# Optimization experiments

Measured on AMD Instinct MI355X. Metric: run time of the kernel, lower is better.

Reference implementation:

```python
import jax, jax.numpy as jnp
import numpy as np

N_NODES = 50000
N_EDGES = 600000
HIDDEN = 128
EDGE_NF = 2          # concat([radial, edge_attr]) -> edges_in_d = 2
NORM_FACTOR = 100.0  # normalization_factor, aggregation 'sum'
NORM_CONSTANT = 1.0


def _lin(key, out_d, in_d):
    # xavier-ish init, (out, in) layout like torch.nn.Linear
    return jax.random.normal(key, (out_d, in_d), jnp.float32) * (1.0 / np.sqrt(in_d))


def setup_inputs() -> dict:
    key = jax.random.key(0)
    ks = iter(jax.random.split(key, 64))
    H = HIDDEN
    inp = {
        "h": jax.random.normal(next(ks), (N_NODES, H), jnp.float32),
        "x": jax.random.normal(next(ks), (N_NODES, 3), jnp.float32),
        "edge_attr": jax.random.normal(next(ks), (N_EDGES, 1), jnp.float32),
        "edge_index": jax.random.randint(next(ks), (2, N_EDGES), 0, N_NODES),
    }
    for i in range(2):  # two GCL layers
        inp[f"g{i}_ew1"] = _lin(next(ks), H, 2 * H + EDGE_NF)
        inp[f"g{i}_eb1"] = jnp.zeros((H,), jnp.float32)
        inp[f"g{i}_ew2"] = _lin(next(ks), H, H)
        inp[f"g{i}_eb2"] = jnp.zeros((H,), jnp.float32)
        inp[f"g{i}_aw"] = _lin(next(ks), 1, H)
        inp[f"g{i}_ab"] = jnp.zeros((1,), jnp.float32)
        inp[f"g{i}_nw1"] = _lin(next(ks), H, 2 * H)
        inp[f"g{i}_nb1"] = jnp.zeros((H,), jnp.float32)
        inp[f"g{i}_nw2"] = _lin(next(ks), H, H)
        inp[f"g{i}_nb2"] = jnp.zeros((H,), jnp.float32)
    inp["eq_w1"] = _lin(next(ks), H, 2 * H + EDGE_NF)
    inp["eq_b1"] = jnp.zeros((H,), jnp.float32)
    inp["eq_w2"] = _lin(next(ks), H, H)
    inp["eq_b2"] = jnp.zeros((H,), jnp.float32)
    inp["eq_w3"] = _lin(next(ks), 1, H)  # bias=False
    return inp


def reference(h, x, edge_attr, edge_index,
              g0_ew1, g0_eb1, g0_ew2, g0_eb2, g0_aw, g0_ab, g0_nw1, g0_nb1, g0_nw2, g0_nb2,
              g1_ew1, g1_eb1, g1_ew2, g1_eb2, g1_aw, g1_ab, g1_nw1, g1_nb1, g1_nw2, g1_nb2,
              eq_w1, eq_b1, eq_w2, eq_b2, eq_w3):
    silu = jax.nn.silu
    row, col = edge_index[0], edge_index[1]
    n = h.shape[0]

    # coord2diff
    diff = x[row] - x[col]                                   # [E, 3]
    radial = jnp.sum(diff * diff, axis=1, keepdims=True)     # [E, 1]
    norm = jnp.sqrt(radial + 1e-8)
    coord_diff = diff / (norm + NORM_CONSTANT)
    ea = jnp.concatenate([radial, edge_attr], axis=1)        # [E, 2]

    gcls = [
        (g0_ew1, g0_eb1, g0_ew2, g0_eb2, g0_aw, g0_ab, g0_nw1, g0_nb1, g0_nw2, g0_nb2),
        (g1_ew1, g1_eb1, g1_ew2, g1_eb2, g1_aw, g1_ab, g1_nw1, g1_nb1, g1_nw2, g1_nb2),
    ]
    for (ew1, eb1, ew2, eb2, aw, ab, nw1, nb1, nw2, nb2) in gcls:
        # edge model: gather -> MLP -> attention gate
        e_in = jnp.concatenate([h[row], h[col], ea], axis=1)  # [E, 2H+2]
        mij = silu(silu(e_in @ ew1.T + eb1) @ ew2.T + eb2)    # [E, H]
        att = jax.nn.sigmoid(mij @ aw.T + ab)                 # [E, 1]
        ef = mij * att
        # node model: scatter-add (sum agg, / normalization_factor)
        agg = jax.ops.segment_sum(ef, row, num_segments=n) / NORM_FACTOR
        msg = silu(jnp.concatenate([h, agg], axis=1) @ nw1.T + nb1) @ nw2.T + nb2
        h = h + msg

    # EquivariantUpdate (tanh=False)
    e_in = jnp.concatenate([h[row], h[col], ea], axis=1)
    s = silu(silu(e_in @ eq_w1.T + eq_b1) @ eq_w2.T + eq_b2) @ eq_w3.T  # [E, 1]
    trans = coord_diff * s                                              # [E, 3]
    x = x + jax.ops.segment_sum(trans, row, num_segments=n) / NORM_FACTOR
    return (h, x)
```

## Files before the change

kernel.cpp:

```cpp
#include <hip/hip_runtime.h>
#include <cmath>

typedef short bfv8 __attribute__((ext_vector_type(8)));
typedef float fv4  __attribute__((ext_vector_type(4)));

#define MFMA_B16(a,b,c) __builtin_amdgcn_mfma_f32_16x16x32_bf16((a),(b),(c),0,0,0)

__device__ __forceinline__ float siluf(float x) { return x / (1.0f + expf(-x)); }

__device__ __forceinline__ unsigned packsplit(float v) {
  unsigned uh = __float_as_uint(v) & 0xffff0000u;
  float lof = v - __uint_as_float(uh);
  return (uh >> 16) | (__float_as_uint(lof) & 0xffff0000u);
}

template <int MODE>
__global__ __launch_bounds__(256, 3)
void edge_mfma(const unsigned short* __restrict__ hhi,
               const unsigned short* __restrict__ hlo,
               const float* __restrict__ radial,
               const float* __restrict__ eattr,
               const int* __restrict__ eidx, int E,
               const unsigned short* __restrict__ w1h, const unsigned short* __restrict__ w1l,
               const float* __restrict__ W1full, const float* __restrict__ b1,
               const unsigned short* __restrict__ w2h, const unsigned short* __restrict__ w2l,
               const float* __restrict__ b2,
               const float* __restrict__ awv, const float* __restrict__ abv,
               const float* __restrict__ xin,
               float* __restrict__ outbuf)
{
  __shared__ int   sRow[128], sCol[128];
  __shared__ float sRad[128], sEa[128];
  __shared__ __align__(16) unsigned sH[4][2048];

  const int tid = threadIdx.x;
  const int w = tid >> 6, l = tid & 63;
  const int c16 = l & 15, g = l >> 4;
  const int e0 = blockIdx.x * 128;

  if (tid < 128) {
    int e = min(e0 + tid, E - 1);
    sRow[tid] = eidx[e];
    sCol[tid] = eidx[E + e];
    sRad[tid] = radial[e];
    sEa[tid]  = eattr[e];
  }
  __syncthreads();

  const int rw = w * 32;
  int nidA[2], nidB[2];
#pragma unroll
  for (int rt = 0; rt < 2; ++rt) {
    nidA[rt] = sRow[rw + rt * 16 + c16];
    nidB[rt] = sCol[rw + rt * 16 + c16];
  }

  fv4 acc[2][8];
#pragma unroll
  for (int a = 0; a < 2; ++a)
#pragma unroll
    for (int b = 0; b < 8; ++b) acc[a][b] = (fv4)0.0f;

#pragma unroll 2
  for (int kc = 0; kc < 8; ++kc) {
    bfv8 Ah[2], Al[2];
    const int kh = (kc & 3) * 32 + g * 8;
#pragma unroll
    for (int rt = 0; rt < 2; ++rt) {
      const int nid = (kc < 4) ? nidA[rt] : nidB[rt];
      const size_t off = (size_t)nid * 128 + kh;
      Ah[rt] = *(const bfv8*)(hhi + off);
      Al[rt] = *(const bfv8*)(hlo + off);
    }
#pragma unroll
    for (int jt = 0; jt < 8; ++jt) {
      const size_t bo = ((size_t)(kc * 8 + jt) * 64 + l) * 8;
      bfv8 Bh = *(const bfv8*)(w1h + bo);
      bfv8 Bl = *(const bfv8*)(w1l + bo);
#pragma unroll
      for (int rt = 0; rt < 2; ++rt) {
        acc[rt][jt] = MFMA_B16(Ah[rt], Bh, acc[rt][jt]);
        acc[rt][jt] = MFMA_B16(Al[rt], Bh, acc[rt][jt]);
        acc[rt][jt] = MFMA_B16(Ah[rt], Bl, acc[rt][jt]);
      }
    }
  }

  unsigned* sHW = sH[w];
  const float ab0 = (MODE == 0) ? abv[0] : 0.0f;

#pragma unroll 1
  for (int rt = 0; rt < 2; ++rt) {
#pragma unroll
    for (int jt = 0; jt < 8; ++jt) {
      const int col = jt * 16 + c16;
      const float wt0 = W1full[(size_t)col * 258 + 256];
      const float wt1 = W1full[(size_t)col * 258 + 257];
      const float bb  = b1[col];
#pragma unroll
      for (int reg = 0; reg < 4; ++reg) {
        const int rr = 4 * g + reg;
        const int er = rw + rt * 16 + rr;
        const float v = acc[rt][jt][reg] + sRad[er] * wt0 + sEa[er] * wt1 + bb;
        sHW[rr * 128 + (col ^ ((rr & 7) << 2))] = packsplit(siluf(v));
      }
    }

    fv4 accB[8];
#pragma unroll
    for (int jt = 0; jt < 8; ++jt) accB[jt] = (fv4)0.0f;
    const int sxz = (c16 & 7) << 2;
#pragma unroll 2
    for (int kc2 = 0; kc2 < 4; ++kc2) {
      const int k0 = kc2 * 32 + g * 8;
      const int i1 = c16 * 128 + (k0 ^ sxz);
      const int4 q0 = *((const int4*)(sHW + i1));
      const int4 q1 = *((const int4*)(sHW + (i1 ^ 4)));
      bfv8 Ah2, Al2;
      {
        const int qq[8] = {q0.x, q0.y, q0.z, q0.w, q1.x, q1.y, q1.z, q1.w};
#pragma unroll
        for (int i = 0; i < 8; ++i) {
          Ah2[i] = (short)(((unsigned)qq[i]) & 0xffffu);
          Al2[i] = (short)(((unsigned)qq[i]) >> 16);
        }
      }
#pragma unroll
      for (int jt = 0; jt < 8; ++jt) {
        const size_t bo = ((size_t)(kc2 * 8 + jt) * 64 + l) * 8;
        bfv8 Bh = *(const bfv8*)(w2h + bo);
        bfv8 Bl = *(const bfv8*)(w2l + bo);
        accB[jt] = MFMA_B16(Ah2, Bh, accB[jt]);
        accB[jt] = MFMA_B16(Al2, Bh, accB[jt]);
        accB[jt] = MFMA_B16(Ah2, Bl, accB[jt]);
      }
    }

    float p[4] = {0.f, 0.f, 0.f, 0.f};
#pragma unroll
    for (int jt = 0; jt < 8; ++jt) {
      const int col = jt * 16 + c16;
      const float bb = b2[col], aa = awv[col];
#pragma unroll
      for (int reg = 0; reg < 4; ++reg) {
        const float m = siluf(accB[jt][reg] + bb);
        accB[jt][reg] = m;
        p[reg] += m * aa;
      }
    }
#pragma unroll
    for (int msk = 1; msk < 16; msk <<= 1) {
#pragma unroll
      for (int reg = 0; reg < 4; ++reg) p[reg] += __shfl_xor(p[reg], msk, 64);
    }

    if constexpr (MODE == 0) {
#pragma unroll
      for (int reg = 0; reg < 4; ++reg) {
        const int er = rw + rt * 16 + 4 * g + reg;
        const int e = e0 + er;
        if (e < E) {
          const float att = 1.0f / (1.0f + expf(-(p[reg] + ab0)));
          float* dst = outbuf + (size_t)sRow[er] * 128;
#pragma unroll
          for (int jt = 0; jt < 8; ++jt)
            unsafeAtomicAdd(dst + jt * 16 + c16, accB[jt][reg] * att);
        }
      }
    } else {
      if (c16 == 0) {
#pragma unroll
        for (int reg = 0; reg < 4; ++reg) {
          const int er = rw + rt * 16 + 4 * g + reg;
          const int e = e0 + er;
          if (e < E) {
            const float s = p[reg] * 0.01f;
            const int nr = sRow[er], nc = sCol[er];
            const float dx = xin[(size_t)nr * 3 + 0] - xin[(size_t)nc * 3 + 0];
            const float dy = xin[(size_t)nr * 3 + 1] - xin[(size_t)nc * 3 + 1];
            const float dz = xin[(size_t)nr * 3 + 2] - xin[(size_t)nc * 3 + 2];
            const float inv = 1.0f / (sqrtf(dx * dx + dy * dy + dz * dz + 1e-8f) + 1.0f);
            unsafeAtomicAdd(outbuf + (size_t)nr * 3 + 0, dx * inv * s);
            unsafeAtomicAdd(outbuf + (size_t)nr * 3 + 1, dy * inv * s);
            unsafeAtomicAdd(outbuf + (size_t)nr * 3 + 2, dz * inv * s);
          }
        }
      }
    }
  }
}

__global__ __launch_bounds__(256, 3)
void node_mfma(float* __restrict__ hio,
               const unsigned short* __restrict__ hhi,
               const unsigned short* __restrict__ hlo,
               const float* __restrict__ agg, int N,
               const unsigned short* __restrict__ w1h, const unsigned short* __restrict__ w1l,
               const float* __restrict__ b1,
               const unsigned short* __restrict__ w2h, const unsigned short* __restrict__ w2l,
               const float* __restrict__ b2)
{
  __shared__ __align__(16) unsigned sH[4][2048];

  const int tid = threadIdx.x;
  const int w = tid >> 6, l = tid & 63;
  const int c16 = l & 15, g = l >> 4;
  const int n0 = blockIdx.x * 128;
  const int rw = w * 32;

  int rowA[2];
#pragma unroll
  for (int rt = 0; rt < 2; ++rt) rowA[rt] = min(n0 + rw + rt * 16 + c16, N - 1);

  fv4 acc[2][8];
#pragma unroll
  for (int a = 0; a < 2; ++a)
#pragma unroll
    for (int b = 0; b < 8; ++b) acc[a][b] = (fv4)0.0f;

#pragma unroll 2
  for (int kc = 0; kc < 8; ++kc) {
    bfv8 Ah[2], Al[2];
    if (kc < 4) {
      const int kh = kc * 32 + g * 8;
#pragma unroll
      for (int rt = 0; rt < 2; ++rt) {
        const size_t off = (size_t)rowA[rt] * 128 + kh;
        Ah[rt] = *(const bfv8*)(hhi + off);
        Al[rt] = *(const bfv8*)(hlo + off);
      }
    } else {
      const int kh = (kc - 4) * 32 + g * 8;
#pragma unroll
      for (int rt = 0; rt < 2; ++rt) {
        const float4 v0 = *(const float4*)(agg + (size_t)rowA[rt] * 128 + kh);
        const float4 v1 = *(const float4*)(agg + (size_t)rowA[rt] * 128 + kh + 4);
        const float vv[8] = {v0.x, v0.y, v0.z, v0.w, v1.x, v1.y, v1.z, v1.w};
#pragma unroll
        for (int i = 0; i < 8; ++i) {
          const float xs = vv[i] * 0.01f;
          const unsigned uh = __float_as_uint(xs) & 0xffff0000u;
          Ah[rt][i] = (short)(uh >> 16);
          const float lof = xs - __uint_as_float(uh);
          Al[rt][i] = (short)(__float_as_uint(lof) >> 16);
        }
      }
    }
#pragma unroll
    for (int jt = 0; jt < 8; ++jt) {
      const size_t bo = ((size_t)(kc * 8 + jt) * 64 + l) * 8;
      bfv8 Bh = *(const bfv8*)(w1h + bo);
      bfv8 Bl = *(const bfv8*)(w1l + bo);
#pragma unroll
      for (int rt = 0; rt < 2; ++rt) {
        acc[rt][jt] = MFMA_B16(Ah[rt], Bh, acc[rt][jt]);
        acc[rt][jt] = MFMA_B16(Al[rt], Bh, acc[rt][jt]);
        acc[rt][jt] = MFMA_B16(Ah[rt], Bl, acc[rt][jt]);
      }
    }
  }

  unsigned* sHW = sH[w];
#pragma unroll 1
  for (int rt = 0; rt < 2; ++rt) {
#pragma unroll
    for (int jt = 0; jt < 8; ++jt) {
      const int col = jt * 16 + c16;
      const float bb = b1[col];
#pragma unroll
      for (int reg = 0; reg < 4; ++reg) {
        const int rr = 4 * g + reg;
        sHW[rr * 128 + (col ^ ((rr & 7) << 2))] = packsplit(siluf(acc[rt][jt][reg] + bb));
      }
    }

    fv4 accB[8];
#pragma unroll
    for (int jt = 0; jt < 8; ++jt) accB[jt] = (fv4)0.0f;
    const int sxz = (c16 & 7) << 2;
#pragma unroll 2
    for (int kc2 = 0; kc2 < 4; ++kc2) {
      const int k0 = kc2 * 32 + g * 8;
      const int i1 = c16 * 128 + (k0 ^ sxz);
      const int4 q0 = *((const int4*)(sHW + i1));
      const int4 q1 = *((const int4*)(sHW + (i1 ^ 4)));
      bfv8 Ah2, Al2;
      {
        const int qq[8] = {q0.x, q0.y, q0.z, q0.w, q1.x, q1.y, q1.z, q1.w};
#pragma unroll
        for (int i = 0; i < 8; ++i) {
          Ah2[i] = (short)(((unsigned)qq[i]) & 0xffffu);
          Al2[i] = (short)(((unsigned)qq[i]) >> 16);
        }
      }
#pragma unroll
      for (int jt = 0; jt < 8; ++jt) {
        const size_t bo = ((size_t)(kc2 * 8 + jt) * 64 + l) * 8;
        bfv8 Bh = *(const bfv8*)(w2h + bo);
        bfv8 Bl = *(const bfv8*)(w2l + bo);
        accB[jt] = MFMA_B16(Ah2, Bh, accB[jt]);
        accB[jt] = MFMA_B16(Al2, Bh, accB[jt]);
        accB[jt] = MFMA_B16(Ah2, Bl, accB[jt]);
      }
    }

#pragma unroll
    for (int reg = 0; reg < 4; ++reg) {
      const int n = n0 + rw + rt * 16 + 4 * g + reg;
      if (n < N) {
        float* hp = hio + (size_t)n * 128;
#pragma unroll
        for (int jt = 0; jt < 8; ++jt) {
          const int col = jt * 16 + c16;
          hp[col] += accB[jt][reg] + b2[col];
        }
      }
    }
  }
}

__global__ void radial_kernel(const float* __restrict__ x,
                              const int* __restrict__ eidx, int E,
                              float* __restrict__ radial)
{
  const int e = blockIdx.x * 256 + threadIdx.x;
  if (e >= E) return;
  const int r = eidx[e], c = eidx[E + e];
  const float dx = x[(size_t)r * 3 + 0] - x[(size_t)c * 3 + 0];
  const float dy = x[(size_t)r * 3 + 1] - x[(size_t)c * 3 + 1];
  const float dz = x[(size_t)r * 3 + 2] - x[(size_t)c * 3 + 2];
  radial[e] = dx * dx + dy * dy + dz * dz;
}

__global__ void split_kernel(const float* __restrict__ src,
                             unsigned short* __restrict__ hi,
                             unsigned short* __restrict__ lo, int n4)
{
  const int i = blockIdx.x * 256 + threadIdx.x;
  if (i >= n4) return;
  const float4 v = ((const float4*)src)[i];
  const float vv[4] = {v.x, v.y, v.z, v.w};
  ushort4 ho, lq;
  unsigned short* hp = (unsigned short*)&ho;
  unsigned short* lp = (unsigned short*)&lq;
#pragma unroll
  for (int k = 0; k < 4; ++k) {
    const unsigned uh = __float_as_uint(vv[k]) & 0xffff0000u;
    hp[k] = (unsigned short)(uh >> 16);
    const float lof = vv[k] - __uint_as_float(uh);
    lp[k] = (unsigned short)(__float_as_uint(lof) >> 16);
  }
  ((ushort4*)hi)[i] = ho;
  ((ushort4*)lo)[i] = lq;
}

struct WDesc { const float* src; unsigned short* hi; unsigned short* lo; int K; int SW; };
struct WAll { WDesc m[10]; };

__global__ void wprep_kernel(WAll wa)
{
  const WDesc d = wa.m[blockIdx.y];
  const int idx = blockIdx.x * 256 + threadIdx.x;
  const int j = idx & 127, k = idx >> 7;
  if (k >= d.K) return;
  const float v = d.src[(size_t)j * d.SW + k];
  const unsigned uh = __float_as_uint(v) & 0xffff0000u;
  const float lof = v - __uint_as_float(uh);
  const int fo = ((((k >> 5) * 8 + (j >> 4)) * 64) + ((k >> 3) & 3) * 16 + (j & 15)) * 8 + (k & 7);
  d.hi[fo] = (unsigned short)(uh >> 16);
  d.lo[fo] = (unsigned short)(__float_as_uint(lof) >> 16);
}

extern "C" void kernel_launch(void* const* d_in, const int* in_sizes, int n_in,
                              void* d_out, int out_size, void* d_ws, size_t ws_size,
                              hipStream_t stream)
{
  const float* h_in  = (const float*)d_in[0];
  const float* x_in  = (const float*)d_in[1];
  const float* eattr = (const float*)d_in[2];
  const int*   eidx  = (const int*)d_in[3];
  const int N = in_sizes[0] / 128;
  const int E = in_sizes[2];

  const float* P[25];
  for (int i = 0; i < 25; ++i) P[i] = (const float*)d_in[4 + i];

  float* h_out = (float*)d_out;
  float* x_out = (float*)d_out + (size_t)N * 128;

  float* radial = (float*)d_ws;
  float* agg    = radial + E;
  unsigned short* hhi = (unsigned short*)(agg + (size_t)N * 128);
  unsigned short* hlo = hhi + (size_t)N * 128;
  unsigned short* wptr = hlo + (size_t)N * 128;

  WAll wa;
  auto addw = [&](int slot, const float* s, int K, int SW) {
    wa.m[slot].src = s; wa.m[slot].hi = wptr; wa.m[slot].lo = wptr + (size_t)K * 128;
    wa.m[slot].K = K; wa.m[slot].SW = SW;
    wptr += (size_t)2 * K * 128;
  };
  addw(0, P[0], 256, 258);  addw(1, P[2], 128, 128);
  addw(2, P[6], 256, 256);  addw(3, P[8], 128, 128);
  addw(4, P[10], 256, 258); addw(5, P[12], 128, 128);
  addw(6, P[16], 256, 256); addw(7, P[18], 128, 128);
  addw(8, P[20], 256, 258); addw(9, P[22], 128, 128);

  hipMemcpyAsync(h_out, h_in, (size_t)N * 128 * sizeof(float),
                 hipMemcpyDeviceToDevice, stream);
  hipMemcpyAsync(x_out, x_in, (size_t)N * 3 * sizeof(float),
                 hipMemcpyDeviceToDevice, stream);

  radial_kernel<<<(E + 255) / 256, 256, 0, stream>>>(x_in, eidx, E, radial);
  wprep_kernel<<<dim3(128, 10), 256, 0, stream>>>(wa);

  const int n4 = N * 32;
  const int sg = (n4 + 255) / 256;
  const int eg = (E + 127) / 128;
  const int ng = (N + 127) / 128;

  for (int lyr = 0; lyr < 2; ++lyr) {
    const float* const* G = P + 10 * lyr;
    const WDesc* M = &wa.m[4 * lyr];
    split_kernel<<<sg, 256, 0, stream>>>(h_out, hhi, hlo, n4);
    hipMemsetAsync(agg, 0, (size_t)N * 128 * sizeof(float), stream);
    edge_mfma<0><<<eg, 256, 0, stream>>>(hhi, hlo, radial, eattr, eidx, E,
        M[0].hi, M[0].lo, G[0], G[1], M[1].hi, M[1].lo, G[3],
        G[4], G[5], nullptr, agg);
    node_mfma<<<ng, 256, 0, stream>>>(h_out, hhi, hlo, agg, N,
        M[2].hi, M[2].lo, G[7], M[3].hi, M[3].lo, G[9]);
  }

  split_kernel<<<sg, 256, 0, stream>>>(h_out, hhi, hlo, n4);
  edge_mfma<1><<<eg, 256, 0, stream>>>(hhi, hlo, radial, eattr, eidx, E,
      wa.m[8].hi, wa.m[8].lo, P[20], P[21], wa.m[9].hi, wa.m[9].lo, P[23],
      P[24], nullptr, x_in, x_out);
}
```

Before: 1.565 ms.

## Sort edges by destination row and pre-reduce messages in LDS before atomics

Adds a counting sort (histogram, scan, scatter) that reorders edges by row, and fuses the radial computation into the scatter step. In the message-passing edge kernel, per-edge messages are staged in shared memory as bf16 pairs, then summed over runs of equal row before any global atomic, so far fewer atomics hit agg. The point is to cut atomic traffic, which dominates the scatter-add. The costs are extra preprocessing kernels, a larger shared-memory footprint with occupancy hint lowered to 2, and bf16 rounding of messages before accumulation, which reduces precision.

```diff
diff --git a/kernel.cpp b/kernel.cpp
--- a/kernel.cpp
+++ b/kernel.cpp
@@ -14,13 +14,73 @@
   return (uh >> 16) | (__float_as_uint(lof) & 0xffff0000u);
 }
 
+__device__ __forceinline__ unsigned bf16rne(float x) {
+  unsigned u = __float_as_uint(x);
+  return (u + 0x7fffu + ((u >> 16) & 1u)) >> 16;
+}
+
+__global__ void hist_kernel(const int* __restrict__ eidx, int E,
+                            unsigned* __restrict__ cnt)
+{
+  const int e = blockIdx.x * 256 + threadIdx.x;
+  if (e < E) atomicAdd(&cnt[eidx[e]], 1u);
+}
+
+__global__ void scan_kernel(const unsigned* __restrict__ cnt,
+                            unsigned* __restrict__ cursor, int N)
+{
+  __shared__ unsigned part[1024];
+  const int t = threadIdx.x;
+  const int chunk = (N + 1023) / 1024;
+  const int base = t * chunk;
+  unsigned s = 0;
+  for (int i = 0; i < chunk; ++i) {
+    const int idx = base + i;
+    if (idx < N) s += cnt[idx];
+  }
+  part[t] = s;
+  __syncthreads();
+  for (int off = 1; off < 1024; off <<= 1) {
+    unsigned v = 0;
+    if (t >= off) v = part[t - off];
+    __syncthreads();
+    if (t >= off) part[t] += v;
+    __syncthreads();
+  }
+  unsigned pre = (t == 0) ? 0u : part[t - 1];
+  for (int i = 0; i < chunk; ++i) {
+    const int idx = base + i;
+    if (idx < N) { cursor[idx] = pre; pre += cnt[idx]; }
+  }
+}
+
+__global__ void scatter_kernel(const float* __restrict__ x,
+                               const int* __restrict__ eidx,
+                               const float* __restrict__ eattr, int E,
+                               unsigned* __restrict__ cursor,
+                               int* __restrict__ sRowA, int* __restrict__ sColA,
+                               float* __restrict__ sRadA, float* __restrict__ sEaA)
+{
+  const int e = blockIdx.x * 256 + threadIdx.x;
+  if (e >= E) return;
+  const int r = eidx[e], c = eidx[E + e];
+  const float dx = x[(size_t)r * 3 + 0] - x[(size_t)c * 3 + 0];
+  const float dy = x[(size_t)r * 3 + 1] - x[(size_t)c * 3 + 1];
+  const float dz = x[(size_t)r * 3 + 2] - x[(size_t)c * 3 + 2];
+  const unsigned pos = atomicAdd(&cursor[r], 1u);
+  sRowA[pos] = r;
+  sColA[pos] = c;
+  sRadA[pos] = dx * dx + dy * dy + dz * dz;
+  sEaA[pos]  = eattr[e];
+}
+
 template <int MODE>
-__global__ __launch_bounds__(256, 3)
+__global__ __launch_bounds__(256, 2)
 void edge_mfma(const unsigned short* __restrict__ hhi,
                const unsigned short* __restrict__ hlo,
-               const float* __restrict__ radial,
-               const float* __restrict__ eattr,
-               const int* __restrict__ eidx, int E,
+               const int* __restrict__ sRowA, const int* __restrict__ sColA,
+               const float* __restrict__ sRadA, const float* __restrict__ sEaA,
+               int E,
                const unsigned short* __restrict__ w1h, const unsigned short* __restrict__ w1l,
                const float* __restrict__ W1full, const float* __restrict__ b1,
                const unsigned short* __restrict__ w2h, const unsigned short* __restrict__ w2l,
@@ -29,9 +89,14 @@
                const float* __restrict__ xin,
                float* __restrict__ outbuf)
 {
-  __shared__ int   sRow[128], sCol[128];
-  __shared__ float sRad[128], sEa[128];
-  __shared__ __align__(16) unsigned sH[4][2048];
+  extern __shared__ __align__(16) char smem[];
+  unsigned* sHall  = (unsigned*)smem;
+  unsigned* sStage = (unsigned*)(smem + 32768);
+  char* ebase = smem + (MODE == 0 ? 65536 : 32768);
+  int*   sRow = (int*)ebase;
+  int*   sCol = sRow + 128;
+  float* sRad = (float*)(sCol + 128);
+  float* sEa  = sRad + 128;
 
   const int tid = threadIdx.x;
   const int w = tid >> 6, l = tid & 63;
@@ -39,11 +104,11 @@
   const int e0 = blockIdx.x * 128;
 
   if (tid < 128) {
-    int e = min(e0 + tid, E - 1);
-    sRow[tid] = eidx[e];
-    sCol[tid] = eidx[E + e];
-    sRad[tid] = radial[e];
-    sEa[tid]  = eattr[e];
+    const int e = min(e0 + tid, E - 1);
+    sRow[tid] = sRowA[e];
+    sCol[tid] = sColA[e];
+    sRad[tid] = sRadA[e];
+    sEa[tid]  = sEaA[e];
   }
   __syncthreads();
 
@@ -86,7 +151,7 @@
     }
   }
 
-  unsigned* sHW = sH[w];
+  unsigned* sHW = sHall + w * 2048;
   const float ab0 = (MODE == 0) ? abv[0] : 0.0f;
 
 #pragma unroll 1
@@ -155,16 +220,22 @@
     }
 
     if constexpr (MODE == 0) {
-#pragma unroll
-      for (int reg = 0; reg < 4; ++reg) {
-        const int er = rw + rt * 16 + 4 * g + reg;
-        const int e = e0 + er;
-        if (e < E) {
-          const float att = 1.0f / (1.0f + expf(-(p[reg] + ab0)));
-          float* dst = outbuf + (size_t)sRow[er] * 128;
-#pragma unroll
-          for (int jt = 0; jt < 8; ++jt)
-            unsafeAtomicAdd(dst + jt * 16 + c16, accB[jt][reg] * att);
+      float att[4];
+#pragma unroll
+      for (int reg = 0; reg < 4; ++reg)
+        att[reg] = 1.0f / (1.0f + expf(-(p[reg] + ab0)));
+#pragma unroll
+      for (int jt = 0; jt < 8; ++jt) {
+#pragma unroll
+        for (int reg = 0; reg < 4; ++reg) {
+          const int er = rw + rt * 16 + 4 * g + reg;
+          float v = (e0 + er < E) ? accB[jt][reg] * att[reg] : 0.0f;
+          const float vn = __shfl_xor(v, 1, 64);
+          if (!(c16 & 1)) {
+            const int cp = jt * 8 + (c16 >> 1);
+            sStage[er * 64 + (cp ^ (((er >> 2) & 3) << 3))] =
+                bf16rne(v) | (bf16rne(vn) << 16);
+          }
         }
       }
     } else {
@@ -188,6 +259,34 @@
       }
     }
   }
+
+  if constexpr (MODE == 0) {
+    __syncthreads();
+    const int cp = tid & 63;
+    const int q  = tid >> 6;
+    const int erb = q * 32;
+    float a0 = 0.0f, a1 = 0.0f;
+    int cur = sRow[erb];
+#pragma unroll 4
+    for (int i = 0; i < 32; ++i) {
+      const int er = erb + i;
+      const int r = sRow[er];
+      if (r != cur) {
+        if (a0 != 0.0f || a1 != 0.0f) {
+          unsafeAtomicAdd(outbuf + (size_t)cur * 128 + 2 * cp,     a0);
+          unsafeAtomicAdd(outbuf + (size_t)cur * 128 + 2 * cp + 1, a1);
+        }
+        cur = r; a0 = 0.0f; a1 = 0.0f;
+      }
+      const unsigned u = sStage[er * 64 + (cp ^ (((er >> 2) & 3) << 3))];
+      a0 += __uint_as_float(u << 16);
+      a1 += __uint_as_float(u & 0xffff0000u);
+    }
+    if (a0 != 0.0f || a1 != 0.0f) {
+      unsafeAtomicAdd(outbuf + (size_t)cur * 128 + 2 * cp,     a0);
+      unsafeAtomicAdd(outbuf + (size_t)cur * 128 + 2 * cp + 1, a1);
+    }
+  }
 }
 
 __global__ __launch_bounds__(256, 3)
@@ -319,19 +418,6 @@
   }
 }
 
-__global__ void radial_kernel(const float* __restrict__ x,
-                              const int* __restrict__ eidx, int E,
-                              float* __restrict__ radial)
-{
-  const int e = blockIdx.x * 256 + threadIdx.x;
-  if (e >= E) return;
-  const int r = eidx[e], c = eidx[E + e];
-  const float dx = x[(size_t)r * 3 + 0] - x[(size_t)c * 3 + 0];
-  const float dy = x[(size_t)r * 3 + 1] - x[(size_t)c * 3 + 1];
-  const float dz = x[(size_t)r * 3 + 2] - x[(size_t)c * 3 + 2];
-  radial[e] = dx * dx + dy * dy + dz * dz;
-}
-
 __global__ void split_kernel(const float* __restrict__ src,
                              unsigned short* __restrict__ hi,
                              unsigned short* __restrict__ lo, int n4)
@@ -388,9 +474,14 @@
   float* h_out = (float*)d_out;
   float* x_out = (float*)d_out + (size_t)N * 128;
 
-  float* radial = (float*)d_ws;
-  float* agg    = radial + E;
-  unsigned short* hhi = (unsigned short*)(agg + (size_t)N * 128);
+  float*    agg    = (float*)d_ws;
+  unsigned* cnt    = (unsigned*)(agg + (size_t)N * 128);
+  unsigned* cursor = cnt + N;
+  int*      sRowA  = (int*)(cursor + N);
+  int*      sColA  = sRowA + E;
+  float*    sRadA  = (float*)(sColA + E);
+  float*    sEaA   = sRadA + E;
+  unsigned short* hhi = (unsigned short*)(sEaA + E);
   unsigned short* hlo = hhi + (size_t)N * 128;
   unsigned short* wptr = hlo + (size_t)N * 128;
 
@@ -411,20 +502,27 @@
   hipMemcpyAsync(x_out, x_in, (size_t)N * 3 * sizeof(float),
                  hipMemcpyDeviceToDevice, stream);
 
-  radial_kernel<<<(E + 255) / 256, 256, 0, stream>>>(x_in, eidx, E, radial);
+  hipMemsetAsync(cnt, 0, (size_t)N * sizeof(unsigned), stream);
+  hist_kernel<<<(E + 255) / 256, 256, 0, stream>>>(eidx, E, cnt);
+  scan_kernel<<<1, 1024, 0, stream>>>(cnt, cursor, N);
+  scatter_kernel<<<(E + 255) / 256, 256, 0, stream>>>(x_in, eidx, eattr, E,
+      cursor, sRowA, sColA, sRadA, sEaA);
+
   wprep_kernel<<<dim3(128, 10), 256, 0, stream>>>(wa);
 
   const int n4 = N * 32;
   const int sg = (n4 + 255) / 256;
   const int eg = (E + 127) / 128;
   const int ng = (N + 127) / 128;
+  const int smem0 = 32768 + 32768 + 2048;
+  const int smem1 = 32768 + 2048;
 
   for (int lyr = 0; lyr < 2; ++lyr) {
     const float* const* G = P + 10 * lyr;
     const WDesc* M = &wa.m[4 * lyr];
     split_kernel<<<sg, 256, 0, stream>>>(h_out, hhi, hlo, n4);
     hipMemsetAsync(agg, 0, (size_t)N * 128 * sizeof(float), stream);
-    edge_mfma<0><<<eg, 256, 0, stream>>>(hhi, hlo, radial, eattr, eidx, E,
+    edge_mfma<0><<<eg, 256, smem0, stream>>>(hhi, hlo, sRowA, sColA, sRadA, sEaA, E,
         M[0].hi, M[0].lo, G[0], G[1], M[1].hi, M[1].lo, G[3],
         G[4], G[5], nullptr, agg);
     node_mfma<<<ng, 256, 0, stream>>>(h_out, hhi, hlo, agg, N,
@@ -432,7 +530,7 @@
   }
 
   split_kernel<<<sg, 256, 0, stream>>>(h_out, hhi, hlo, n4);
-  edge_mfma<1><<<eg, 256, 0, stream>>>(hhi, hlo, radial, eattr, eidx, E,
+  edge_mfma<1><<<eg, 256, smem1, stream>>>(hhi, hlo, sRowA, sColA, sRadA, sEaA, E,
       wa.m[8].hi, wa.m[8].lo, P[20], P[21], wa.m[9].hi, wa.m[9].lo, P[23],
       P[24], nullptr, x_in, x_out);
 }
```

Result: slower. 1.698 ms (+8.6%).
